# Kernel tuning notes

Hardware: AMD Instinct MI355X
Metric: run time of the kernel (lower is better)

Reference implementation:

```python
import jax, jax.numpy as jnp
import numpy as np

EPS = 1e-5
SLOPE = 0.2

def lrelu(x):
    return jnp.where(x >= 0, x, SLOPE * x)

def conv3(x, w):
    # 3x3 conv, stride 1, padding 1, NCHW / OIHW
    return jax.lax.conv_general_dilated(x, w, (1, 1), ((1, 1), (1, 1)),
                                        dimension_numbers=('NCHW', 'OIHW', 'NCHW'))

def bn(x, g, b, m, v):
    # eval-mode BatchNorm2d with running stats
    scale = g / jnp.sqrt(v + EPS)
    return x * scale[None, :, None, None] + (b - m * scale)[None, :, None, None]

def up2_bilinear(x):
    # UpsamplingBilinear2d(scale_factor=2) => align_corners=True, separable interp
    B, C, H, W = x.shape
    def axis_interp(a, n, axis):
        co = jnp.linspace(0.0, n - 1.0, 2 * n)
        i0 = jnp.floor(co).astype(jnp.int32)
        i1 = jnp.minimum(i0 + 1, n - 1)
        w1 = co - i0.astype(co.dtype)
        a0 = jnp.take(a, i0, axis=axis)
        a1 = jnp.take(a, i1, axis=axis)
        shp = [1, 1, 1, 1]; shp[axis] = 2 * n
        w1 = w1.reshape(shp)
        return a0 * (1.0 - w1) + a1 * w1
    x = axis_interp(x, H, 2)
    x = axis_interp(x, W, 3)
    return x

def self_attention(x, Wq, bq, Wk, bk, Wv, bv):
    B, C, H, W = x.shape
    N = H * W
    xf = x.reshape(B, C, N)                                    # [B,C,N]
    q = jnp.einsum('oc,bcn->bno', Wq, xf) + bq                 # [B,N,C/2]
    k = jnp.einsum('oc,bcn->bon', Wk, xf) + bk[None, :, None]  # [B,C/2,N]
    v = jnp.einsum('oc,bcn->bon', Wv, xf) + bv[None, :, None]  # [B,C,N]
    attn = jax.nn.softmax(jnp.einsum('bno,bom->bnm', q, k), axis=-1)  # [B,N,N]
    out = jnp.einsum('bcn,bmn->bcm', v, attn)                  # [B,C,N]
    return out.reshape(B, C, H, W) + x

def setup_inputs():
    key = jax.random.key(0)
    ks = jax.random.split(key, 8)
    B, Cin, Cout, H, W = 4, 256, 128, 32, 32
    s = 0.05
    f32 = jnp.float32
    return {
        'x': jax.random.normal(ks[0], (B, Cin, H, W), f32),
        'W_up': jax.random.normal(ks[1], (Cout, Cin, 3, 3), f32) * s,
        'b_up': jnp.zeros((Cout,), f32),
        'g0': jnp.ones((Cout,), f32), 'be0': jnp.zeros((Cout,), f32),
        'm0': jnp.zeros((Cout,), f32), 'v0': jnp.ones((Cout,), f32),
        'W_r0': jax.random.normal(ks[2], (Cout, Cout, 3, 3), f32) * s,
        'g1': jnp.ones((Cout,), f32), 'be1': jnp.zeros((Cout,), f32),
        'm1': jnp.zeros((Cout,), f32), 'v1': jnp.ones((Cout,), f32),
        'W_r1': jax.random.normal(ks[3], (Cout, Cout, 3, 3), f32) * s,
        'g2': jnp.ones((Cout,), f32), 'be2': jnp.zeros((Cout,), f32),
        'm2': jnp.zeros((Cout,), f32), 'v2': jnp.ones((Cout,), f32),
        'Wq': jax.random.normal(ks[4], (Cout // 2, Cout), f32) * s,
        'bq': jnp.zeros((Cout // 2,), f32),
        'Wk': jax.random.normal(ks[5], (Cout // 2, Cout), f32) * s,
        'bk': jnp.zeros((Cout // 2,), f32),
        'Wv': jax.random.normal(ks[6], (Cout, Cout), f32) * s,
        'bv': jnp.zeros((Cout,), f32),
    }

def reference(x, W_up, b_up, g0, be0, m0, v0, W_r0, g1, be1, m1, v1,
              W_r1, g2, be2, m2, v2, Wq, bq, Wk, bk, Wv, bv):
    out = up2_bilinear(x)
    out = conv3(out, W_up) + b_up[None, :, None, None]
    out = lrelu(bn(out, g0, be0, m0, v0))
    identity = out
    out = lrelu(bn(conv3(out, W_r0), g1, be1, m1, v1))
    out = lrelu(bn(conv3(out, W_r1), g2, be2, m2, v2))
    out = self_attention(out, Wq, bq, Wk, bk, Wv, bv)
    out = out + identity
    return lrelu(out)
```

## Files before the change

kernel.cpp:

```cpp
#include <hip/hip_runtime.h>
#include <math.h>

#define EPS 1e-5f
#define SLOPE 0.2f

typedef unsigned short u16;
typedef unsigned int u32;
typedef __attribute__((ext_vector_type(4))) float f32x4;
typedef __attribute__((ext_vector_type(16))) float f32x16;
typedef __attribute__((ext_vector_type(8))) short s16x8;
typedef __attribute__((ext_vector_type(4))) short s16x4;
typedef __attribute__((ext_vector_type(4))) u32 u32x4;

__device__ __forceinline__ float lrelu(float x){ return x >= 0.f ? x : SLOPE*x; }

__device__ __forceinline__ u16 f2b(float x){
  u32 u = __float_as_uint(x);
  u32 r = (u + 0x7FFFu + ((u >> 16) & 1u)) >> 16;
  return (u16)r;
}
__device__ __forceinline__ float b2f(short v){
  return __uint_as_float(((u32)(u16)v) << 16);
}
__device__ __forceinline__ u32 swz(u32 a){ return a ^ (((a>>9)&7u)<<4); }

__global__ void k_tr(const float* __restrict__ x, u16* __restrict__ xh){
  __shared__ float t[32][33];
  int b = blockIdx.x>>8; int c0 = ((blockIdx.x>>5)&7)*32; int p0 = (blockIdx.x&31)*32;
  int tx = threadIdx.x&31, ty = threadIdx.x>>5;
  #pragma unroll
  for(int r=0;r<32;r+=8)
    t[ty+r][tx] = x[((size_t)(b*256 + c0+ty+r))*1024 + p0 + tx];
  __syncthreads();
  #pragma unroll
  for(int r=0;r<32;r+=8)
    xh[((size_t)(b*1024 + p0+ty+r))*256 + c0 + tx] = f2b(t[tx][ty+r]);
}

__global__ void k_up8(const u16* __restrict__ xh, u16* __restrict__ u){
  int idx = blockIdx.x*256 + threadIdx.x;
  int cg = idx & 31;
  int ow = (idx>>5) & 63; int oh = (idx>>11)&63; int b = idx>>17;
  const float st = 31.0f/63.0f;
  float fh = oh*st, fw = ow*st;
  int h0=(int)fh, w0=(int)fw;
  float wh = fh-(float)h0, ww = fw-(float)w0;
  int h1=min(h0+1,31), w1=min(w0+1,31);
  const u16* xb = xh + ((size_t)b*1024)*256 + cg*8;
  s16x8 a = *(const s16x8*)(xb + (size_t)(h0*32+w0)*256);
  s16x8 bb= *(const s16x8*)(xb + (size_t)(h0*32+w1)*256);
  s16x8 c = *(const s16x8*)(xb + (size_t)(h1*32+w0)*256);
  s16x8 d = *(const s16x8*)(xb + (size_t)(h1*32+w1)*256);
  u16 o[8];
  #pragma unroll
  for(int j=0;j<8;++j){
    float top = b2f(a[j]) + (b2f(bb[j])-b2f(a[j]))*ww;
    float bot = b2f(c[j]) + (b2f(d[j])-b2f(c[j]))*ww;
    o[j] = f2b(top + (bot-top)*wh);
  }
  *(s16x8*)(u + (size_t)idx*8) = *(s16x8*)o;
}

__global__ void k_wall(const float* __restrict__ W_up, const float* __restrict__ W_r0,
                       const float* __restrict__ W_r1, const float* __restrict__ Wq,
                       const float* __restrict__ Wk, const float* __restrict__ Wv,
                       u16* __restrict__ wtu, u16* __restrict__ wtr0,
                       u16* __restrict__ wtr1, u16* __restrict__ wqk,
                       u16* __restrict__ wv){
  int idx = blockIdx.x*256 + threadIdx.x;
  if(idx < 294912){
    int ci = idx&255, t2 = idx>>8; int tap = t2%9, co = t2/9;
    wtu[idx] = f2b(W_up[((size_t)co*256+ci)*9 + tap]);
  } else if(idx < 442368){
    int i2 = idx - 294912;
    int ci = i2&127, t2 = i2>>7; int tap = t2%9, co = t2/9;
    wtr0[i2] = f2b(W_r0[((size_t)co*128+ci)*9 + tap]);
  } else if(idx < 589824){
    int i2 = idx - 442368;
    int ci = i2&127, t2 = i2>>7; int tap = t2%9, co = t2/9;
    wtr1[i2] = f2b(W_r1[((size_t)co*128+ci)*9 + tap]);
  } else if(idx < 606208){
    int i2 = idx - 589824;
    wqk[i2] = f2b(i2 < 8192 ? Wq[i2] : Wk[i2-8192]);
  } else {
    int i2 = idx - 606208;
    wv[i2] = f2b(Wv[i2]);
  }
}

template<int CIN>
__global__ __launch_bounds__(128) void k_cmfma(
    const u16* __restrict__ xin, const u16* __restrict__ wt,
    const float* __restrict__ bias,
    const float* __restrict__ g, const float* __restrict__ be,
    const float* __restrict__ mm, const float* __restrict__ vv,
    u16* __restrict__ out)
{
  constexpr int K = CIN*9;
  int blk = blockIdx.x;
  int mt = blk & 63;
  int nt = (blk>>6) & 1;
  int b  = blk >> 7;
  int wid = threadIdx.x>>6, lane = threadIdx.x&63;
  int gq = lane>>4, lr = lane&15;
  int g8 = gq*8;
  int mb = mt*64 + wid*32;
  int h = mb>>6, w0 = mb&63;
  int cob = nt*64;

  f32x4 acc[2][4];
  #pragma unroll
  for(int pf=0;pf<2;++pf)
    #pragma unroll
    for(int cf=0;cf<4;++cf) acc[pf][cf]=(f32x4)0.f;

  const u16* xb = xin + (size_t)b*4096*CIN;
  const u16* wr = wt + (size_t)(cob+lr)*K + g8;

  for(int dy=-1; dy<=1; ++dy){
    int hh = h+dy;
    if(hh<0 || hh>63) continue;
    #pragma unroll
    for(int dx=-1; dx<=1; ++dx){
      int tap = (dy+1)*3 + (dx+1);
      const u16* wtap = wr + tap*CIN;
      const u16* ar[2]; bool av[2];
      #pragma unroll
      for(int pf=0;pf<2;++pf){
        int ww = w0 + pf*16 + lr + dx;
        av[pf] = (ww>=0)&&(ww<64);
        int wc = ww<0?0:(ww>63?63:ww);
        ar[pf] = xb + ((size_t)hh*64 + wc)*CIN + g8;
      }
      #pragma unroll
      for(int kc=0;kc<CIN/32;++kc){
        s16x8 af[2];
        #pragma unroll
        for(int pf=0;pf<2;++pf){
          s16x8 t = *(const s16x8*)(ar[pf] + kc*32);
          af[pf] = av[pf] ? t : (s16x8)0;
        }
        s16x8 bfr[4];
        #pragma unroll
        for(int cf=0;cf<4;++cf)
          bfr[cf] = *(const s16x8*)(wtap + (size_t)cf*16*K + kc*32);
        #pragma unroll
        for(int pf=0;pf<2;++pf)
          #pragma unroll
          for(int cf=0;cf<4;++cf)
            acc[pf][cf] = __builtin_amdgcn_mfma_f32_16x16x32_bf16(af[pf], bfr[cf], acc[pf][cf],0,0,0);
      }
    }
  }
  #pragma unroll
  for(int cf=0;cf<4;++cf){
    int co = cob + cf*16 + lr;
    float sc = g[co]*rsqrtf(vv[co]+EPS);
    float sh = be[co] - mm[co]*sc;
    if(bias) sh += bias[co]*sc;
    #pragma unroll
    for(int pf=0;pf<2;++pf){
      #pragma unroll
      for(int r=0;r<4;++r){
        int pix = mb + pf*16 + gq*4 + r;
        float v_ = acc[pf][cf][r]*sc + sh;
        out[((size_t)b*4096 + pix)*128 + co] = f2b(lrelu(v_));
      }
    }
  }
}

__global__ __launch_bounds__(128) void k_projqk(
  const u16* __restrict__ x2b, const u16* __restrict__ wqk,
  const float* __restrict__ bq, const float* __restrict__ bk,
  u16* __restrict__ qbf, u16* __restrict__ kbf)
{
  int blk = blockIdx.x;
  int nt = blk & 1;
  int mt = blk >> 1;
  int wid = threadIdx.x>>6, lane = threadIdx.x&63;
  int gq=lane>>4, lr=lane&15, g8=gq*8;
  int mb = mt*64 + wid*32;
  int cob = nt*64;
  f32x4 acc[2][4];
  #pragma unroll
  for(int pf=0;pf<2;++pf)
    #pragma unroll
    for(int cf=0;cf<4;++cf) acc[pf][cf]=(f32x4)0.f;
  const u16* xr0 = x2b + (size_t)(mb+lr)*128 + g8;
  const u16* xr1 = x2b + (size_t)(mb+16+lr)*128 + g8;
  const u16* wr  = wqk + (size_t)(cob+lr)*128 + g8;
  #pragma unroll
  for(int kc=0;kc<4;++kc){
    s16x8 a0 = *(const s16x8*)(xr0 + kc*32);
    s16x8 a1 = *(const s16x8*)(xr1 + kc*32);
    s16x8 bfr[4];
    #pragma unroll
    for(int cf=0;cf<4;++cf) bfr[cf] = *(const s16x8*)(wr + (size_t)cf*16*128 + kc*32);
    #pragma unroll
    for(int cf=0;cf<4;++cf){
      acc[0][cf] = __builtin_amdgcn_mfma_f32_16x16x32_bf16(a0, bfr[cf], acc[0][cf],0,0,0);
      acc[1][cf] = __builtin_amdgcn_mfma_f32_16x16x32_bf16(a1, bfr[cf], acc[1][cf],0,0,0);
    }
  }
  #pragma unroll
  for(int cf=0;cf<4;++cf){
    int co = cob + cf*16 + lr;
    float bi = co<64 ? bq[co] : bk[co-64];
    #pragma unroll
    for(int pf=0;pf<2;++pf){
      #pragma unroll
      for(int r=0;r<4;++r){
        int pix = mb + pf*16 + gq*4 + r;
        float v_ = acc[pf][cf][r] + bi;
        if(co<64) qbf[(size_t)pix*64 + co] = f2b(v_);
        else      kbf[(size_t)pix*64 + (co-64)] = f2b(v_);
      }
    }
  }
}

__global__ __launch_bounds__(128) void k_projv(
  const u16* __restrict__ x2b, const u16* __restrict__ wv,
  const float* __restrict__ bv, u16* __restrict__ vbf)
{
  int blk = blockIdx.x;
  int cot = blk & 3;
  int pt  = (blk>>2) & 31;
  int b   = blk >> 7;
  int wid = threadIdx.x>>6, lane = threadIdx.x&63;
  int gq=lane>>4, lr=lane&15, g8=gq*8;
  int cb = cot*32;
  int nb = pt*128 + wid*64;
  f32x4 acc[2][4];
  #pragma unroll
  for(int pf=0;pf<2;++pf)
    #pragma unroll
    for(int cf=0;cf<4;++cf) acc[pf][cf]=(f32x4)0.f;
  const u16* ar0 = wv + (size_t)(cb+lr)*128 + g8;
  const u16* ar1 = wv + (size_t)(cb+16+lr)*128 + g8;
  const u16* xr  = x2b + ((size_t)b*4096 + nb + lr)*128 + g8;
  #pragma unroll
  for(int kc=0;kc<4;++kc){
    s16x8 a0 = *(const s16x8*)(ar0+kc*32);
    s16x8 a1 = *(const s16x8*)(ar1+kc*32);
    s16x8 bfr[4];
    #pragma unroll
    for(int cf=0;cf<4;++cf) bfr[cf] = *(const s16x8*)(xr + (size_t)cf*16*128 + kc*32);
    #pragma unroll
    for(int cf=0;cf<4;++cf){
      acc[0][cf] = __builtin_amdgcn_mfma_f32_16x16x32_bf16(a0, bfr[cf], acc[0][cf],0,0,0);
      acc[1][cf] = __builtin_amdgcn_mfma_f32_16x16x32_bf16(a1, bfr[cf], acc[1][cf],0,0,0);
    }
  }
  #pragma unroll
  for(int pf=0;pf<2;++pf){
    #pragma unroll
    for(int r=0;r<4;++r){
      int co = cb + pf*16 + gq*4 + r;
      float bi = bv[co];
      #pragma unroll
      for(int cf=0;cf<4;++cf){
        int pix = nb + cf*16 + lr;
        vbf[((size_t)b*128+co)*4096 + pix] = f2b(acc[pf][cf][r] + bi);
      }
    }
  }
}

__global__ __launch_bounds__(512, 2) void k_fattn4(
    const u16* __restrict__ qbf, const u16* __restrict__ kbf,
    const u16* __restrict__ vbf, const u16* __restrict__ x2b,
    const u16* __restrict__ idbb, float* __restrict__ out){
  __shared__ char lds[2*49152 + 2048];
  float* sst = (float*)(lds + 2*49152);
  int tid = threadIdx.x;
  int wid = tid>>6, lane = tid&63;
  int ml = lane&31, hi = lane>>5;
  int g  = wid&1;
  int s  = wid>>1;
  int blk = blockIdx.x;
  int b  = blk&3;
  int mt = ((blk>>3)<<1) | ((blk>>2)&1);
  int mbase = mt*64 + g*32;

  const u16* qp = qbf + ((size_t)b*4096 + mbase + ml)*64 + hi*8;
  s16x8 qf[4];
  #pragma unroll
  for(int kc=0;kc<4;++kc) qf[kc] = *(const s16x8*)(qp + kc*16);

  const u16* sgp[6]; u32 sdo[6];
  #pragma unroll
  for(int i=0;i<2;++i){
    int id = i*512 + tid;
    int st = id>>8, r = (id>>3)&31, c = id&7;
    sgp[i] = kbf + (size_t)b*262144 + (size_t)(st*32 + r)*64 + c*8;
    sdo[i] = swz(st*4096 + ((u32)((c>>1)*64 + (c&1)*32 + r) << 4));
  }
  #pragma unroll
  for(int i=2;i<6;++i){
    int q2 = (i-2)*512 + tid;
    int st = q2>>9, w = q2&511, row = w>>2, d = w&3;
    sgp[i] = vbf + ((size_t)b*128 + row)*4096 + st*32 + d*8;
    sdo[i] = swz(16384 + st*8192 + ((u32)((((row>>5)<<1) + (d>>1))*64 + (d&1)*32 + (row&31)) << 4));
  }

  f32x16 acc[4];
  #pragma unroll
  for(int cb=0;cb<4;++cb) acc[cb] = (f32x16)0.f;
  float mrun = -3.0e38f, lrun = 0.f;

  s16x8 stg[6];
  #pragma unroll
  for(int i=0;i<2;++i) stg[i] = *(const s16x8*)(sgp[i]);
  #pragma unroll
  for(int i=2;i<6;++i) stg[i] = *(const s16x8*)(sgp[i]);
  #pragma unroll
  for(int i=0;i<6;++i) *(s16x8*)(lds + sdo[i]) = stg[i];
  __syncthreads();

  for(int j=0;j<32;++j){
    int p = j&1;
    if(j<31){
      #pragma unroll
      for(int i=0;i<2;++i) stg[i] = *(const s16x8*)(sgp[i] + (size_t)(j+1)*8192);
      #pragma unroll
      for(int i=2;i<6;++i) stg[i] = *(const s16x8*)(sgp[i] + (size_t)(j+1)*128);
    }
    char* Kb = lds + p*49152 + s*4096;
    char* Vb = lds + p*49152 + 16384 + s*8192;
    f32x16 sv = (f32x16)0.f;
    __builtin_amdgcn_s_setprio(1);
    #pragma unroll
    for(int kc=0;kc<4;++kc){
      s16x8 ka = *(const s16x8*)(Kb + swz((u32)((kc*64+lane)<<4)));
      sv = __builtin_amdgcn_mfma_f32_32x32x16_bf16(ka, qf[kc], sv, 0, 0, 0);
    }
    __builtin_amdgcn_s_setprio(0);
    float tm = sv[0];
    #pragma unroll
    for(int r=1;r<16;++r) tm = fmaxf(tm, sv[r]);
    tm = fmaxf(tm, __shfl_xor(tm, 32));
    if(__any(tm > mrun + 8.f)){
      float mnew = fmaxf(mrun, tm);
      float alpha = __expf(mrun - mnew);
      lrun *= alpha;
      #pragma unroll
      for(int cb=0;cb<4;++cb)
        #pragma unroll
        for(int r=0;r<16;++r) acc[cb][r] *= alpha;
      mrun = mnew;
    }
    float ps = 0.f;
    #pragma unroll
    for(int r=0;r<16;++r){ float pv = __expf(sv[r] - mrun); sv[r] = pv; ps += pv; }
    ps += __shfl_xor(ps, 32);
    lrun += ps;
    u32 pk[8];
    #pragma unroll
    for(int i=0;i<8;++i){
      u32 w_;
      asm("v_cvt_pk_bf16_f32 %0, %1, %2" : "=v"(w_) : "v"(sv[2*i]), "v"(sv[2*i+1]));
      pk[i] = w_;
    }
    asm volatile("v_permlane32_swap_b32 %0, %1" : "+v"(pk[0]), "+v"(pk[2]));
    asm volatile("v_permlane32_swap_b32 %0, %1" : "+v"(pk[1]), "+v"(pk[3]));
    asm volatile("v_permlane32_swap_b32 %0, %1" : "+v"(pk[4]), "+v"(pk[6]));
    asm volatile("v_permlane32_swap_b32 %0, %1" : "+v"(pk[5]), "+v"(pk[7]));
    u32x4 w0 = {pk[0], pk[1], pk[2], pk[3]};
    u32x4 w1 = {pk[4], pk[5], pk[6], pk[7]};
    s16x8 pb0 = __builtin_bit_cast(s16x8, w0);
    s16x8 pb1 = __builtin_bit_cast(s16x8, w1);
    __builtin_amdgcn_s_setprio(1);
    #pragma unroll
    for(int cb=0;cb<4;++cb){
      s16x8 va0 = *(const s16x8*)(Vb + swz((u32)(((cb*2+0)*64+lane)<<4)));
      s16x8 va1 = *(const s16x8*)(Vb + swz((u32)(((cb*2+1)*64+lane)<<4)));
      acc[cb] = __builtin_amdgcn_mfma_f32_32x32x16_bf16(va0, pb0, acc[cb], 0, 0, 0);
      acc[cb] = __builtin_amdgcn_mfma_f32_32x32x16_bf16(va1, pb1, acc[cb], 0, 0, 0);
    }
    __builtin_amdgcn_s_setprio(0);
    if(j<31){
      #pragma unroll
      for(int i=0;i<6;++i) *(s16x8*)(lds + (p^1)*49152 + sdo[i]) = stg[i];
    }
    __syncthreads();
  }

  if(hi == 0){
    sst[wid*64 + ml*2 + 0] = mrun;
    sst[wid*64 + ml*2 + 1] = lrun;
  }
  __syncthreads();
  float mws[4], sws[4], Mx = -3.0e38f;
  #pragma unroll
  for(int s2=0;s2<4;++s2){ mws[s2] = sst[(s2*2+g)*64 + ml*2 + 0]; Mx = fmaxf(Mx, mws[s2]); }
  float lstar = 0.f;
  #pragma unroll
  for(int s2=0;s2<4;++s2){ sws[s2] = __expf(mws[s2]-Mx); lstar += sst[(s2*2+g)*64 + ml*2 + 1]*sws[s2]; }
  float inv = 1.f/lstar;
  int m = mbase + ml;

  float* dump = (float*)lds;
  #pragma unroll
  for(int cb=0;cb<4;++cb){
    #pragma unroll
    for(int r=0;r<16;++r)
      dump[wid*1024 + r*64 + lane] = acc[cb][r];
    __syncthreads();
    int c0 = cb*32 + s*8 + 4*hi;
    size_t rbase = ((size_t)b*4096 + m)*128 + c0;
    s16x4 xr = *(const s16x4*)(x2b + rbase);
    s16x4 ir = *(const s16x4*)(idbb + rbase);
    #pragma unroll
    for(int q=0;q<4;++q){
      int r = s*4 + q;
      float O = 0.f;
      #pragma unroll
      for(int s2=0;s2<4;++s2) O += sws[s2]*dump[(s2*2+g)*1024 + r*64 + lane];
      float val = O*inv + b2f(xr[q]) + b2f(ir[q]);
      out[((size_t)b*128 + c0 + q)*4096 + m] = lrelu(val);
    }
    __syncthreads();
  }
}

extern "C" void kernel_launch(void* const* d_in, const int* in_sizes, int n_in,
                              void* d_out, int out_size, void* d_ws, size_t ws_size,
                              hipStream_t stream) {
  const float* x    = (const float*)d_in[0];
  const float* W_up = (const float*)d_in[1];
  const float* b_up = (const float*)d_in[2];
  const float* g0   = (const float*)d_in[3];
  const float* be0  = (const float*)d_in[4];
  const float* m0   = (const float*)d_in[5];
  const float* v0   = (const float*)d_in[6];
  const float* W_r0 = (const float*)d_in[7];
  const float* g1   = (const float*)d_in[8];
  const float* be1  = (const float*)d_in[9];
  const float* m1   = (const float*)d_in[10];
  const float* v1   = (const float*)d_in[11];
  const float* W_r1 = (const float*)d_in[12];
  const float* g2   = (const float*)d_in[13];
  const float* be2  = (const float*)d_in[14];
  const float* m2   = (const float*)d_in[15];
  const float* v2   = (const float*)d_in[16];
  const float* Wq   = (const float*)d_in[17];
  const float* bq   = (const float*)d_in[18];
  const float* Wk   = (const float*)d_in[19];
  const float* bk   = (const float*)d_in[20];
  const float* Wv   = (const float*)d_in[21];
  const float* bv   = (const float*)d_in[22];

  float* ws = (float*)d_ws;
  u16* xh   = (u16*)(ws + 0);
  u16* ub   = (u16*)(ws + 524288);
  u16* idbb = (u16*)(ws + 2621440);
  u16* x1b  = (u16*)(ws + 3670016);
  u16* x2b  = (u16*)(ws + 4718592);
  u16* qbf  = (u16*)(ws + 5767168);
  u16* kbf  = (u16*)(ws + 6291456);
  u16* vbf  = (u16*)(ws + 6815744);
  u16* wtu  = (u16*)(ws + 7864320);
  u16* wtr0 = (u16*)(ws + 8011776);
  u16* wtr1 = (u16*)(ws + 8085504);
  u16* wqk  = (u16*)(ws + 8159232);
  u16* wvb  = (u16*)(ws + 8167424);
  float* out = (float*)d_out;

  k_wall<<<2432, 256, 0, stream>>>(W_up, W_r0, W_r1, Wq, Wk, Wv, wtu, wtr0, wtr1, wqk, wvb);
  k_tr<<<1024, 256, 0, stream>>>(x, xh);
  k_up8<<<2048, 256, 0, stream>>>(xh, ub);
  k_cmfma<256><<<512, 128, 0, stream>>>(ub, wtu, b_up, g0, be0, m0, v0, idbb);
  k_cmfma<128><<<512, 128, 0, stream>>>(idbb, wtr0, nullptr, g1, be1, m1, v1, x1b);
  k_cmfma<128><<<512, 128, 0, stream>>>(x1b, wtr1, nullptr, g2, be2, m2, v2, x2b);
  k_projqk<<<512, 128, 0, stream>>>(x2b, wqk, bq, bk, qbf, kbf);
  k_projv<<<512, 128, 0, stream>>>(x2b, wvb, bv, vbf);
  k_fattn4<<<256, 512, 0, stream>>>(qbf, kbf, vbf, x2b, idbb, out);
}
```

Before: 178.0 us.

## Switch activations and weights to channel-blocked layout of 32-channel chunks

Activations move from pixel-major with all channels contiguous to [batch][channel-chunk of 32][pixel][32], and conv/projection weights to [kchunk][tap][cout][32]. Every producer and consumer kernel (transpose, upsample, weight prep, convs, Q/K/V projections, attention epilogue) is updated to the new indexing. The aim is denser 64-byte rows per MFMA fragment load and better cache locality for the weight and input reads in the implicit-GEMM conv. The cost is more complex address arithmetic, and every kernel must agree on the layout.

Measured after the change: 143.5 us. 19.4% less time.

```diff
diff --git a/kernel.cpp b/kernel.cpp
--- a/kernel.cpp
+++ b/kernel.cpp
@@ -26,31 +26,34 @@
 
 __global__ void k_tr(const float* __restrict__ x, u16* __restrict__ xh){
   __shared__ float t[32][33];
-  int b = blockIdx.x>>8; int c0 = ((blockIdx.x>>5)&7)*32; int p0 = (blockIdx.x&31)*32;
+  int b = blockIdx.x>>8; int kc = (blockIdx.x>>5)&7; int p0 = (blockIdx.x&31)*32;
   int tx = threadIdx.x&31, ty = threadIdx.x>>5;
   #pragma unroll
   for(int r=0;r<32;r+=8)
-    t[ty+r][tx] = x[((size_t)(b*256 + c0+ty+r))*1024 + p0 + tx];
+    t[ty+r][tx] = x[((size_t)(b*256 + kc*32+ty+r))*1024 + p0 + tx];
   __syncthreads();
   #pragma unroll
   for(int r=0;r<32;r+=8)
-    xh[((size_t)(b*1024 + p0+ty+r))*256 + c0 + tx] = f2b(t[tx][ty+r]);
+    xh[((size_t)((b*8+kc)*1024) + p0+ty+r)*32 + tx] = f2b(t[tx][ty+r]);
 }
 
 __global__ void k_up8(const u16* __restrict__ xh, u16* __restrict__ u){
   int idx = blockIdx.x*256 + threadIdx.x;
-  int cg = idx & 31;
-  int ow = (idx>>5) & 63; int oh = (idx>>11)&63; int b = idx>>17;
+  int sub = (idx&3)*8;
+  int pix = (idx>>2)&4095;
+  int kc  = (idx>>14)&7;
+  int b   = idx>>17;
+  int ow = pix&63, oh = pix>>6;
   const float st = 31.0f/63.0f;
   float fh = oh*st, fw = ow*st;
   int h0=(int)fh, w0=(int)fw;
   float wh = fh-(float)h0, ww = fw-(float)w0;
   int h1=min(h0+1,31), w1=min(w0+1,31);
-  const u16* xb = xh + ((size_t)b*1024)*256 + cg*8;
-  s16x8 a = *(const s16x8*)(xb + (size_t)(h0*32+w0)*256);
-  s16x8 bb= *(const s16x8*)(xb + (size_t)(h0*32+w1)*256);
-  s16x8 c = *(const s16x8*)(xb + (size_t)(h1*32+w0)*256);
-  s16x8 d = *(const s16x8*)(xb + (size_t)(h1*32+w1)*256);
+  const u16* xb = xh + (size_t)((b*8+kc)*1024)*32 + sub;
+  s16x8 a = *(const s16x8*)(xb + (size_t)(h0*32+w0)*32);
+  s16x8 bb= *(const s16x8*)(xb + (size_t)(h0*32+w1)*32);
+  s16x8 c = *(const s16x8*)(xb + (size_t)(h1*32+w0)*32);
+  s16x8 d = *(const s16x8*)(xb + (size_t)(h1*32+w1)*32);
   u16 o[8];
   #pragma unroll
   for(int j=0;j<8;++j){
@@ -58,7 +61,7 @@
     float bot = b2f(c[j]) + (b2f(d[j])-b2f(c[j]))*ww;
     o[j] = f2b(top + (bot-top)*wh);
   }
-  *(s16x8*)(u + (size_t)idx*8) = *(s16x8*)o;
+  *(s16x8*)(u + (size_t)((b*8+kc)*4096 + pix)*32 + sub) = *(s16x8*)o;
 }
 
 __global__ void k_wall(const float* __restrict__ W_up, const float* __restrict__ W_r0,
@@ -69,22 +72,27 @@
                        u16* __restrict__ wv){
   int idx = blockIdx.x*256 + threadIdx.x;
   if(idx < 294912){
-    int ci = idx&255, t2 = idx>>8; int tap = t2%9, co = t2/9;
-    wtu[idx] = f2b(W_up[((size_t)co*256+ci)*9 + tap]);
+    int ci = idx&31, co = (idx>>5)&127, t2 = idx>>12;
+    int tap = t2%9, kc = t2/9;
+    wtu[idx] = f2b(W_up[((size_t)co*256 + kc*32+ci)*9 + tap]);
   } else if(idx < 442368){
     int i2 = idx - 294912;
-    int ci = i2&127, t2 = i2>>7; int tap = t2%9, co = t2/9;
-    wtr0[i2] = f2b(W_r0[((size_t)co*128+ci)*9 + tap]);
+    int ci = i2&31, co = (i2>>5)&127, t2 = i2>>12;
+    int tap = t2%9, kc = t2/9;
+    wtr0[i2] = f2b(W_r0[((size_t)co*128 + kc*32+ci)*9 + tap]);
   } else if(idx < 589824){
     int i2 = idx - 442368;
-    int ci = i2&127, t2 = i2>>7; int tap = t2%9, co = t2/9;
-    wtr1[i2] = f2b(W_r1[((size_t)co*128+ci)*9 + tap]);
+    int ci = i2&31, co = (i2>>5)&127, t2 = i2>>12;
+    int tap = t2%9, kc = t2/9;
+    wtr1[i2] = f2b(W_r1[((size_t)co*128 + kc*32+ci)*9 + tap]);
   } else if(idx < 606208){
     int i2 = idx - 589824;
-    wqk[i2] = f2b(i2 < 8192 ? Wq[i2] : Wk[i2-8192]);
+    int ci = i2&31, o = (i2>>5)&127, kc = i2>>12;
+    wqk[i2] = f2b(o < 64 ? Wq[(size_t)o*128 + kc*32+ci] : Wk[(size_t)(o-64)*128 + kc*32+ci]);
   } else {
     int i2 = idx - 606208;
-    wv[i2] = f2b(Wv[i2]);
+    int ci = i2&31, c = (i2>>5)&127, kc = i2>>12;
+    wv[i2] = f2b(Wv[(size_t)c*128 + kc*32+ci]);
   }
 }
 
@@ -96,7 +104,7 @@
     const float* __restrict__ mm, const float* __restrict__ vv,
     u16* __restrict__ out)
 {
-  constexpr int K = CIN*9;
+  constexpr int KC = CIN/32;
   int blk = blockIdx.x;
   int mt = blk & 63;
   int nt = (blk>>6) & 1;
@@ -114,8 +122,7 @@
     #pragma unroll
     for(int cf=0;cf<4;++cf) acc[pf][cf]=(f32x4)0.f;
 
-  const u16* xb = xin + (size_t)b*4096*CIN;
-  const u16* wr = wt + (size_t)(cob+lr)*K + g8;
+  const u16* xb = xin + (size_t)b*KC*4096*32;
 
   for(int dy=-1; dy<=1; ++dy){
     int hh = h+dy;
@@ -123,27 +130,27 @@
     #pragma unroll
     for(int dx=-1; dx<=1; ++dx){
       int tap = (dy+1)*3 + (dx+1);
-      const u16* wtap = wr + tap*CIN;
       const u16* ar[2]; bool av[2];
       #pragma unroll
       for(int pf=0;pf<2;++pf){
         int ww = w0 + pf*16 + lr + dx;
         av[pf] = (ww>=0)&&(ww<64);
         int wc = ww<0?0:(ww>63?63:ww);
-        ar[pf] = xb + ((size_t)hh*64 + wc)*CIN + g8;
+        ar[pf] = xb + ((size_t)(hh*64 + wc))*32 + g8;
       }
       #pragma unroll
-      for(int kc=0;kc<CIN/32;++kc){
+      for(int kc=0;kc<KC;++kc){
         s16x8 af[2];
         #pragma unroll
         for(int pf=0;pf<2;++pf){
-          s16x8 t = *(const s16x8*)(ar[pf] + kc*32);
+          s16x8 t = *(const s16x8*)(ar[pf] + (size_t)kc*131072);
           af[pf] = av[pf] ? t : (s16x8)0;
         }
+        const u16* wtap = wt + ((size_t)((kc*9+tap)*128) + cob + lr)*32 + g8;
         s16x8 bfr[4];
         #pragma unroll
         for(int cf=0;cf<4;++cf)
-          bfr[cf] = *(const s16x8*)(wtap + (size_t)cf*16*K + kc*32);
+          bfr[cf] = *(const s16x8*)(wtap + cf*16*32);
         #pragma unroll
         for(int pf=0;pf<2;++pf)
           #pragma unroll
@@ -158,13 +165,14 @@
     float sc = g[co]*rsqrtf(vv[co]+EPS);
     float sh = be[co] - mm[co]*sc;
     if(bias) sh += bias[co]*sc;
+    int kco = co>>5, ci = co&31;
     #pragma unroll
     for(int pf=0;pf<2;++pf){
       #pragma unroll
       for(int r=0;r<4;++r){
         int pix = mb + pf*16 + gq*4 + r;
         float v_ = acc[pf][cf][r]*sc + sh;
-        out[((size_t)b*4096 + pix)*128 + co] = f2b(lrelu(v_));
+        out[((size_t)((b*4 + kco)*4096) + pix)*32 + ci] = f2b(lrelu(v_));
       }
     }
   }
@@ -180,23 +188,23 @@
   int mt = blk >> 1;
   int wid = threadIdx.x>>6, lane = threadIdx.x&63;
   int gq=lane>>4, lr=lane&15, g8=gq*8;
-  int mb = mt*64 + wid*32;
+  int gp = mt*64 + wid*32;
+  int b = gp>>12, p = gp&4095;
   int cob = nt*64;
   f32x4 acc[2][4];
   #pragma unroll
   for(int pf=0;pf<2;++pf)
     #pragma unroll
     for(int cf=0;cf<4;++cf) acc[pf][cf]=(f32x4)0.f;
-  const u16* xr0 = x2b + (size_t)(mb+lr)*128 + g8;
-  const u16* xr1 = x2b + (size_t)(mb+16+lr)*128 + g8;
-  const u16* wr  = wqk + (size_t)(cob+lr)*128 + g8;
+  const u16* xb = x2b + (size_t)b*4*4096*32;
   #pragma unroll
   for(int kc=0;kc<4;++kc){
-    s16x8 a0 = *(const s16x8*)(xr0 + kc*32);
-    s16x8 a1 = *(const s16x8*)(xr1 + kc*32);
+    s16x8 a0 = *(const s16x8*)(xb + ((size_t)(kc*4096) + p + lr)*32 + g8);
+    s16x8 a1 = *(const s16x8*)(xb + ((size_t)(kc*4096) + p + 16 + lr)*32 + g8);
     s16x8 bfr[4];
     #pragma unroll
-    for(int cf=0;cf<4;++cf) bfr[cf] = *(const s16x8*)(wr + (size_t)cf*16*128 + kc*32);
+    for(int cf=0;cf<4;++cf)
+      bfr[cf] = *(const s16x8*)(wqk + ((size_t)(kc*128) + cob + cf*16 + lr)*32 + g8);
     #pragma unroll
     for(int cf=0;cf<4;++cf){
       acc[0][cf] = __builtin_amdgcn_mfma_f32_16x16x32_bf16(a0, bfr[cf], acc[0][cf],0,0,0);
@@ -211,7 +219,7 @@
     for(int pf=0;pf<2;++pf){
       #pragma unroll
       for(int r=0;r<4;++r){
-        int pix = mb + pf*16 + gq*4 + r;
+        int pix = gp + pf*16 + gq*4 + r;
         float v_ = acc[pf][cf][r] + bi;
         if(co<64) qbf[(size_t)pix*64 + co] = f2b(v_);
         else      kbf[(size_t)pix*64 + (co-64)] = f2b(v_);
@@ -237,16 +245,15 @@
   for(int pf=0;pf<2;++pf)
     #pragma unroll
     for(int cf=0;cf<4;++cf) acc[pf][cf]=(f32x4)0.f;
-  const u16* ar0 = wv + (size_t)(cb+lr)*128 + g8;
-  const u16* ar1 = wv + (size_t)(cb+16+lr)*128 + g8;
-  const u16* xr  = x2b + ((size_t)b*4096 + nb + lr)*128 + g8;
+  const u16* xb = x2b + (size_t)b*4*4096*32;
   #pragma unroll
   for(int kc=0;kc<4;++kc){
-    s16x8 a0 = *(const s16x8*)(ar0+kc*32);
-    s16x8 a1 = *(const s16x8*)(ar1+kc*32);
+    s16x8 a0 = *(const s16x8*)(wv + ((size_t)(kc*128) + cb + lr)*32 + g8);
+    s16x8 a1 = *(const s16x8*)(wv + ((size_t)(kc*128) + cb + 16 + lr)*32 + g8);
     s16x8 bfr[4];
     #pragma unroll
-    for(int cf=0;cf<4;++cf) bfr[cf] = *(const s16x8*)(xr + (size_t)cf*16*128 + kc*32);
+    for(int cf=0;cf<4;++cf)
+      bfr[cf] = *(const s16x8*)(xb + ((size_t)(kc*4096) + nb + cf*16 + lr)*32 + g8);
     #pragma unroll
     for(int cf=0;cf<4;++cf){
       acc[0][cf] = __builtin_amdgcn_mfma_f32_16x16x32_bf16(a0, bfr[cf], acc[0][cf],0,0,0);
@@ -409,9 +416,9 @@
       dump[wid*1024 + r*64 + lane] = acc[cb][r];
     __syncthreads();
     int c0 = cb*32 + s*8 + 4*hi;
-    size_t rbase = ((size_t)b*4096 + m)*128 + c0;
-    s16x4 xr = *(const s16x4*)(x2b + rbase);
-    s16x4 ir = *(const s16x4*)(idbb + rbase);
+    size_t rb2 = ((size_t)((b*4 + cb)*4096) + m)*32 + s*8 + 4*hi;
+    s16x4 xr = *(const s16x4*)(x2b + rb2);
+    s16x4 ir = *(const s16x4*)(idbb + rb2);
     #pragma unroll
     for(int q=0;q<4;++q){
       int r = s*4 + q;
```
